# Optimization experiments

Hardware: AMD Instinct MI355X
Metric: run time of the kernel (lower is better)

The kernel has to match this reference:

```python
import jax, jax.numpy as jnp
import numpy as np

NODE_NUM = 100000
LAYER_NUM = 4
EMB = 128
FEAT = 256
BATCH = 4096
NEIGH = 32
EPS = 1e-12  # F.normalize default eps


def setup_inputs() -> dict:
    key = jax.random.key(0)
    ks = jax.random.split(key, 10)
    std = 1.0 / np.sqrt(EMB)
    return {
        "layers": jax.random.randint(ks[0], (BATCH,), 0, LAYER_NUM),
        "node_i": jax.random.randint(ks[1], (BATCH,), 0, NODE_NUM),
        "neighs_i": jax.random.randint(ks[2], (BATCH, LAYER_NUM, NEIGH), 0, NODE_NUM),
        "features": jax.random.normal(ks[3], (NODE_NUM, FEAT), dtype=jnp.float32),
        "layer_embs": jax.random.uniform(ks[4], (NODE_NUM, LAYER_NUM, EMB), dtype=jnp.float32, minval=-1.0, maxval=1.0),
        "neigh_emb_trans": jax.random.normal(ks[5], (LAYER_NUM, FEAT, EMB), dtype=jnp.float32) * std,
        "trans_weights": jax.random.normal(ks[6], (EMB, EMB), dtype=jnp.float32) * std,
        "trans_weights_s1": jax.random.normal(ks[7], (EMB, EMB), dtype=jnp.float32) * std,
        "trans_weights_s2": jax.random.normal(ks[8], (EMB, 1), dtype=jnp.float32) * std,
    }


def reference(layers, node_i, neighs_i, features, layer_embs, neigh_emb_trans,
              trans_weights, trans_weights_s1, trans_weights_s2):
    # Gather neighbor features: [B, L, J, F]
    feats_n = features[neighs_i]
    # Per-layer linear transform == diagonal of torch's 'bijk,akm->bijam' over (i,a):
    # [B, L, J, M]
    h = jnp.einsum('bljf,lfm->bljm', feats_n, neigh_emb_trans)
    # Sum over neighbors -> [B, L, M]
    h = h.sum(axis=2)
    # Attention over layers: tanh(h @ Ws1) @ Ws2 -> [B, L]
    scores = jnp.squeeze(jnp.tanh(h @ trans_weights_s1) @ trans_weights_s2, axis=-1)
    att = jax.nn.softmax(scores, axis=1)  # [B, L]
    # Attention-weighted layer aggregation -> [B, M]
    agg = jnp.einsum('bl,blm->bm', att, h)
    node_embed = agg @ trans_weights  # [B, M]
    final = node_embed + layer_embs[node_i, layers]  # residual with per-(node,layer) emb
    # F.normalize(dim=1): x / max(||x||_2, eps)
    norm = jnp.linalg.norm(final, axis=1, keepdims=True)
    return final / jnp.maximum(norm, EPS)
```

## Files before the change

### kernel.cpp

```cpp
#include <hip/hip_runtime.h>
#include <hip/hip_bf16.h>
#include <math.h>

#define BATCH 4096
#define LNUM  4
#define NEIGH 32
#define FEAT  256
#define EMB   128

#define B_TILE 8
#define ROWS   (B_TILE * LNUM)

__global__ __launch_bounds__(256) void fused_liamne(
    const int* __restrict__ layers, const int* __restrict__ node_i,
    const int* __restrict__ neighs, const float* __restrict__ features,
    const float* __restrict__ layer_embs, const float* __restrict__ W,
    const float* __restrict__ Wt, const float* __restrict__ Ws1,
    const float* __restrict__ Ws2, float* __restrict__ out) {
  __shared__ float sS[ROWS][FEAT];
  __shared__ float sH[ROWS][EMB];
  __shared__ float sc[ROWS];

  int b0 = blockIdx.x * B_TILE;
  int tid = threadIdx.x;
  int w = tid >> 6;
  int lane = tid & 63;

#pragma unroll
  for (int i = 0; i < 8; ++i) {
    int r = w * 8 + i;
    int lb = r >> 2, l = r & 3;
    const int* nbr = neighs + ((size_t)(b0 + lb) * LNUM + l) * NEIGH;
    int myn = nbr[lane & 31];
    float ax = 0.f, ay = 0.f, az = 0.f, aw = 0.f;
#pragma unroll 8
    for (int j = 0; j < NEIGH; ++j) {
      int n = __shfl(myn, j, 64);
      float4 v = ((const float4*)(features + (size_t)n * FEAT))[lane];
      ax += v.x; ay += v.y; az += v.z; aw += v.w;
    }
    ((float4*)sS[r])[lane] = make_float4(ax, ay, az, aw);
  }
  __syncthreads();

  {
    const float* Wl = W + (size_t)w * FEAT * EMB;
    float acc[8][2] = {};
    for (int k = 0; k < FEAT; k += 4) {
      float4 s[8];
#pragma unroll
      for (int lb = 0; lb < 8; ++lb)
        s[lb] = *(const float4*)&sS[lb * 4 + w][k];
#pragma unroll
      for (int kk = 0; kk < 4; ++kk) {
        float2 wv = *(const float2*)&Wl[(size_t)(k + kk) * EMB + lane * 2];
#pragma unroll
        for (int lb = 0; lb < 8; ++lb) {
          float sv = ((const float*)&s[lb])[kk];
          acc[lb][0] += sv * wv.x;
          acc[lb][1] += sv * wv.y;
        }
      }
    }
#pragma unroll
    for (int lb = 0; lb < 8; ++lb)
      *(float2*)&sH[lb * 4 + w][lane * 2] = make_float2(acc[lb][0], acc[lb][1]);
  }
  __syncthreads();

  {
    float acc[8][2] = {};
    for (int k = 0; k < EMB; k += 4) {
      float4 h[8];
#pragma unroll
      for (int i = 0; i < 8; ++i)
        h[i] = *(const float4*)&sH[w * 8 + i][k];
#pragma unroll
      for (int kk = 0; kk < 4; ++kk) {
        float2 wv = *(const float2*)&Ws1[(size_t)(k + kk) * EMB + lane * 2];
#pragma unroll
        for (int i = 0; i < 8; ++i) {
          float hv = ((const float*)&h[i])[kk];
          acc[i][0] += hv * wv.x;
          acc[i][1] += hv * wv.y;
        }
      }
    }
    float2 w2 = *(const float2*)&Ws2[lane * 2];
#pragma unroll
    for (int i = 0; i < 8; ++i) {
      float p = tanhf(acc[i][0]) * w2.x + tanhf(acc[i][1]) * w2.y;
#pragma unroll
      for (int m = 1; m < 64; m <<= 1) p += __shfl_xor(p, m, 64);
      if (lane == 0) sc[w * 8 + i] = p;
    }
  }
  __syncthreads();

  float* sAgg = &sS[0][0];
  for (int i = tid; i < B_TILE * EMB; i += 256) {
    int lb = i >> 7, m = i & 127;
    float s0 = sc[lb * 4 + 0], s1 = sc[lb * 4 + 1];
    float s2 = sc[lb * 4 + 2], s3 = sc[lb * 4 + 3];
    float mx = fmaxf(fmaxf(s0, s1), fmaxf(s2, s3));
    float e0 = expf(s0 - mx), e1 = expf(s1 - mx);
    float e2 = expf(s2 - mx), e3 = expf(s3 - mx);
    float inv = 1.0f / (e0 + e1 + e2 + e3);
    float a = e0 * sH[lb * 4 + 0][m] + e1 * sH[lb * 4 + 1][m] +
              e2 * sH[lb * 4 + 2][m] + e3 * sH[lb * 4 + 3][m];
    sAgg[i] = a * inv;
  }
  __syncthreads();

  {
    int g = tid >> 5;
    int t = tid & 31;
    float ax = 0.f, ay = 0.f, az = 0.f, aw = 0.f;
    for (int k = 0; k < EMB; ++k) {
      float4 wv = ((const float4*)(Wt + (size_t)k * EMB))[t];
      float a = sAgg[g * EMB + k];
      ax += a * wv.x; ay += a * wv.y; az += a * wv.z; aw += a * wv.w;
    }
    int b = b0 + g;
    int node = node_i[b];
    int lay = layers[b];
    float4 e =
        ((const float4*)(layer_embs + ((size_t)node * LNUM + lay) * EMB))[t];
    ax += e.x; ay += e.y; az += e.z; aw += e.w;
    float ss = ax * ax + ay * ay + az * az + aw * aw;
#pragma unroll
    for (int m = 1; m < 32; m <<= 1) ss += __shfl_xor(ss, m, 64);
    float inv = 1.0f / fmaxf(sqrtf(ss), 1e-12f);
    ((float4*)(out + (size_t)b * EMB))[t] =
        make_float4(ax * inv, ay * inv, az * inv, aw * inv);
  }
}

extern "C" void kernel_launch(void* const* d_in, const int* in_sizes, int n_in,
                              void* d_out, int out_size, void* d_ws,
                              size_t ws_size, hipStream_t stream) {
  const int* layers = (const int*)d_in[0];
  const int* node_i = (const int*)d_in[1];
  const int* neighs = (const int*)d_in[2];
  const float* features = (const float*)d_in[3];
  const float* layer_embs = (const float*)d_in[4];
  const float* neigh_emb_trans = (const float*)d_in[5];
  const float* trans_weights = (const float*)d_in[6];
  const float* trans_weights_s1 = (const float*)d_in[7];
  const float* trans_weights_s2 = (const float*)d_in[8];
  float* out = (float*)d_out;

  fused_liamne<<<dim3(BATCH / B_TILE), 256, 0, stream>>>(
      layers, node_i, neighs, features, layer_embs, neigh_emb_trans,
      trans_weights, trans_weights_s1, trans_weights_s2, out);
}
```

Measured before the change: 404.7 us.

## Halve batch tile and batch 16 independent neighbor gathers per wave

The batch tile drops from 8 to 4, doubling the block count and halving shared memory per block, and the launch bounds now request 4 blocks per CU for higher occupancy. The neighbor-gather phase is rewritten so each wave handles one batch element across all 4 layers and issues 16 independent feature loads before accumulating, which raises memory-level parallelism on the gather. The later phases are remapped to the smaller tile, with one wave per batch row in the final projection. In exchange, weight matrices are re-read from cache by twice as many blocks, and the extra in-flight loads raise register pressure.

After: 397.9 us. No clear change (-1.7%).

```diff
diff --git a/kernel.cpp b/kernel.cpp
--- a/kernel.cpp
+++ b/kernel.cpp
@@ -8,10 +8,10 @@
 #define FEAT  256
 #define EMB   128
 
-#define B_TILE 8
+#define B_TILE 4
 #define ROWS   (B_TILE * LNUM)
 
-__global__ __launch_bounds__(256) void fused_liamne(
+__global__ __launch_bounds__(256, 4) void fused_liamne(
     const int* __restrict__ layers, const int* __restrict__ node_i,
     const int* __restrict__ neighs, const float* __restrict__ features,
     const float* __restrict__ layer_embs, const float* __restrict__ W,
@@ -26,36 +26,54 @@
   int w = tid >> 6;
   int lane = tid & 63;
 
+  {
+    int nIdx[LNUM];
 #pragma unroll
-  for (int i = 0; i < 8; ++i) {
-    int r = w * 8 + i;
-    int lb = r >> 2, l = r & 3;
-    const int* nbr = neighs + ((size_t)(b0 + lb) * LNUM + l) * NEIGH;
-    int myn = nbr[lane & 31];
-    float ax = 0.f, ay = 0.f, az = 0.f, aw = 0.f;
-#pragma unroll 8
-    for (int j = 0; j < NEIGH; ++j) {
-      int n = __shfl(myn, j, 64);
-      float4 v = ((const float4*)(features + (size_t)n * FEAT))[lane];
-      ax += v.x; ay += v.y; az += v.z; aw += v.w;
+    for (int l = 0; l < LNUM; ++l) {
+      const int* nbr = neighs + ((size_t)(b0 + w) * LNUM + l) * NEIGH;
+      nIdx[l] = nbr[lane & 31];
     }
-    ((float4*)sS[r])[lane] = make_float4(ax, ay, az, aw);
+    const float4* f4 = (const float4*)features;
+    float4 acc[LNUM];
+#pragma unroll
+    for (int l = 0; l < LNUM; ++l) acc[l] = make_float4(0.f, 0.f, 0.f, 0.f);
+#pragma unroll
+    for (int jj = 0; jj < 8; ++jj) {
+      float4 v[LNUM][4];
+#pragma unroll
+      for (int l = 0; l < LNUM; ++l)
+#pragma unroll
+        for (int q = 0; q < 4; ++q) {
+          int n = __shfl(nIdx[l], jj * 4 + q, 64);
+          v[l][q] = f4[(size_t)n * (FEAT / 4) + lane];
+        }
+#pragma unroll
+      for (int l = 0; l < LNUM; ++l)
+#pragma unroll
+        for (int q = 0; q < 4; ++q) {
+          acc[l].x += v[l][q].x; acc[l].y += v[l][q].y;
+          acc[l].z += v[l][q].z; acc[l].w += v[l][q].w;
+        }
+    }
+#pragma unroll
+    for (int l = 0; l < LNUM; ++l)
+      ((float4*)sS[w * LNUM + l])[lane] = acc[l];
   }
   __syncthreads();
 
   {
     const float* Wl = W + (size_t)w * FEAT * EMB;
-    float acc[8][2] = {};
+    float acc[B_TILE][2] = {};
     for (int k = 0; k < FEAT; k += 4) {
-      float4 s[8];
+      float4 s[B_TILE];
 #pragma unroll
-      for (int lb = 0; lb < 8; ++lb)
-        s[lb] = *(const float4*)&sS[lb * 4 + w][k];
+      for (int lb = 0; lb < B_TILE; ++lb)
+        s[lb] = *(const float4*)&sS[lb * LNUM + w][k];
 #pragma unroll
       for (int kk = 0; kk < 4; ++kk) {
         float2 wv = *(const float2*)&Wl[(size_t)(k + kk) * EMB + lane * 2];
 #pragma unroll
-        for (int lb = 0; lb < 8; ++lb) {
+        for (int lb = 0; lb < B_TILE; ++lb) {
           float sv = ((const float*)&s[lb])[kk];
           acc[lb][0] += sv * wv.x;
           acc[lb][1] += sv * wv.y;
@@ -63,23 +81,24 @@
       }
     }
 #pragma unroll
-    for (int lb = 0; lb < 8; ++lb)
-      *(float2*)&sH[lb * 4 + w][lane * 2] = make_float2(acc[lb][0], acc[lb][1]);
+    for (int lb = 0; lb < B_TILE; ++lb)
+      *(float2*)&sH[lb * LNUM + w][lane * 2] =
+          make_float2(acc[lb][0], acc[lb][1]);
   }
   __syncthreads();
 
   {
-    float acc[8][2] = {};
+    float acc[4][2] = {};
     for (int k = 0; k < EMB; k += 4) {
-      float4 h[8];
+      float4 h[4];
 #pragma unroll
-      for (int i = 0; i < 8; ++i)
-        h[i] = *(const float4*)&sH[w * 8 + i][k];
+      for (int i = 0; i < 4; ++i)
+        h[i] = *(const float4*)&sH[w * 4 + i][k];
 #pragma unroll
       for (int kk = 0; kk < 4; ++kk) {
         float2 wv = *(const float2*)&Ws1[(size_t)(k + kk) * EMB + lane * 2];
 #pragma unroll
-        for (int i = 0; i < 8; ++i) {
+        for (int i = 0; i < 4; ++i) {
           float hv = ((const float*)&h[i])[kk];
           acc[i][0] += hv * wv.x;
           acc[i][1] += hv * wv.y;
@@ -88,11 +107,11 @@
     }
     float2 w2 = *(const float2*)&Ws2[lane * 2];
 #pragma unroll
-    for (int i = 0; i < 8; ++i) {
+    for (int i = 0; i < 4; ++i) {
       float p = tanhf(acc[i][0]) * w2.x + tanhf(acc[i][1]) * w2.y;
 #pragma unroll
       for (int m = 1; m < 64; m <<= 1) p += __shfl_xor(p, m, 64);
-      if (lane == 0) sc[w * 8 + i] = p;
+      if (lane == 0) sc[w * 4 + i] = p;
     }
   }
   __syncthreads();
@@ -113,26 +132,26 @@
   __syncthreads();
 
   {
-    int g = tid >> 5;
-    int t = tid & 31;
-    float ax = 0.f, ay = 0.f, az = 0.f, aw = 0.f;
+    float ax = 0.f, ay = 0.f;
     for (int k = 0; k < EMB; ++k) {
-      float4 wv = ((const float4*)(Wt + (size_t)k * EMB))[t];
-      float a = sAgg[g * EMB + k];
-      ax += a * wv.x; ay += a * wv.y; az += a * wv.z; aw += a * wv.w;
+      float2 wv = *(const float2*)&Wt[(size_t)k * EMB + lane * 2];
+      float a = sAgg[w * EMB + k];
+      ax += a * wv.x;
+      ay += a * wv.y;
     }
-    int b = b0 + g;
+    int b = b0 + w;
     int node = node_i[b];
     int lay = layers[b];
-    float4 e =
-        ((const float4*)(layer_embs + ((size_t)node * LNUM + lay) * EMB))[t];
-    ax += e.x; ay += e.y; az += e.z; aw += e.w;
-    float ss = ax * ax + ay * ay + az * az + aw * aw;
+    float2 e = *(const float2*)&layer_embs[((size_t)node * LNUM + lay) * EMB +
+                                           lane * 2];
+    ax += e.x;
+    ay += e.y;
+    float ss = ax * ax + ay * ay;
 #pragma unroll
-    for (int m = 1; m < 32; m <<= 1) ss += __shfl_xor(ss, m, 64);
+    for (int m = 1; m < 64; m <<= 1) ss += __shfl_xor(ss, m, 64);
     float inv = 1.0f / fmaxf(sqrtf(ss), 1e-12f);
-    ((float4*)(out + (size_t)b * EMB))[t] =
-        make_float4(ax * inv, ay * inv, az * inv, aw * inv);
+    *(float2*)&out[(size_t)b * EMB + lane * 2] =
+        make_float2(ax * inv, ay * inv);
   }
 }
 
```
